# Performance work log

Hardware: AMD Instinct MI355X
Metric: run time of the kernel (lower is better)

Reference implementation:

```python
import jax, jax.numpy as jnp
import numpy as np

NUM_ATOMS = 4_000_000
NUM_TYPES = 11

def setup_inputs() -> dict:
    key = jax.random.key(0)
    k1, k2 = jax.random.split(key)
    input_coords = jax.random.normal(k1, (3 * NUM_ATOMS,), dtype=jnp.float32)
    atom_types = jax.random.randint(k2, (NUM_ATOMS,), 0, NUM_TYPES, dtype=jnp.int64)
    return {"input_coords": input_coords, "atom_types": atom_types, "num_atom_types": NUM_TYPES}

def reference(input_coords, atom_types, num_atom_types):
    # counts per atom type  [T]
    counts = jnp.bincount(atom_types, length=num_atom_types).astype(jnp.int32)
    # exclusive prefix sum -> bucket offsets  [T]
    offsets = (jnp.cumsum(counts) - counts).astype(jnp.int32)
    # stable sort by type reproduces the C++ bucket fill order:
    # atoms of the same type keep their original relative order.
    perm = jnp.argsort(atom_types, stable=True)  # [N] source index for each output slot
    coords3 = input_coords.reshape(-1, 3)        # [N,3]
    typed_coords = coords3[perm].reshape(-1)     # [3N] type-grouped flat coords
    return typed_coords, counts, offsets
```

## Files before the change

kernel.cpp:

```cpp
#include <hip/hip_runtime.h>

#define NTYPES 11
#define BLOCK  256
#define ITEMS  8
#define CHUNK  (BLOCK * ITEMS)
#define MAXCH  32

__global__ __launch_bounds__(BLOCK) void hist_kernel(
    const int* __restrict__ types, int N, int B, int* __restrict__ bc) {
  __shared__ int shCnt[NTYPES];
  const int tid = threadIdx.x;
  const int b = blockIdx.x;
  if (tid < NTYPES) shCnt[tid] = 0;
  __syncthreads();

  const int run = b * CHUNK + tid * ITEMS;
  int cnt[NTYPES];
#pragma unroll
  for (int t = 0; t < NTYPES; ++t) cnt[t] = 0;

  if (run < N) {
    const int4* p = (const int4*)(types + run);
    int4 a0 = p[0], a1 = p[1];
    int ty[ITEMS] = {a0.x, a0.y, a0.z, a0.w, a1.x, a1.y, a1.z, a1.w};
#pragma unroll
    for (int k = 0; k < ITEMS; ++k) {
#pragma unroll
      for (int t = 0; t < NTYPES; ++t) cnt[t] += (ty[k] == t) ? 1 : 0;
    }
  }

  const int lane = tid & 63;
#pragma unroll
  for (int t = 0; t < NTYPES; ++t) {
    int v = cnt[t];
    for (int o = 32; o >= 1; o >>= 1) v += __shfl_down(v, o);
    if (lane == 0) atomicAdd(&shCnt[t], v);
  }
  __syncthreads();
  if (tid < NTYPES) bc[tid * B + b] = shCnt[tid];
}

__global__ __launch_bounds__(NTYPES * 64) void scan_kernel(
    const int* __restrict__ bc, int B, int* __restrict__ scanOut,
    int* __restrict__ offs, float* __restrict__ outTail) {
  __shared__ int totals[NTYPES];
  const int lane = threadIdx.x & 63;
  const int t = threadIdx.x >> 6;
  const int nch = (B + 63) >> 6;

  int x[MAXCH];
#pragma unroll
  for (int c = 0; c < MAXCH; ++c) {
    const int idx = c * 64 + lane;
    x[c] = (c < nch && idx < B) ? bc[t * B + idx] : 0;
  }

  int carry = 0;
#pragma unroll
  for (int c = 0; c < MAXCH; ++c) {
    if (c >= nch) break;
    int incl = x[c];
#pragma unroll
    for (int o = 1; o < 64; o <<= 1) {
      int v = __shfl_up(incl, o);
      if (lane >= o) incl += v;
    }
    incl += carry;
    const int idx = c * 64 + lane;
    if (idx < B) scanOut[t * B + idx] = incl - x[c];
    carry = __shfl(incl, 63);
  }
  if (lane == 0) totals[t] = carry;
  __syncthreads();

  if (threadIdx.x == 0) {
    int off = 0;
    for (int u = 0; u < NTYPES; ++u) {
      const int c = totals[u];
      offs[u] = off;
      outTail[u] = (float)c;
      outTail[NTYPES + u] = (float)off;
      off += c;
    }
  }
}

__global__ __launch_bounds__(BLOCK) void scatter_kernel(
    const float* __restrict__ coords, const int* __restrict__ types,
    const int* __restrict__ scanOut, const int* __restrict__ offs, int N,
    int B, float* __restrict__ out) {
  __shared__ float shC[CHUNK * 3];
  __shared__ int wtot[NTYPES][4];
  __shared__ int shOff[NTYPES + 1];
  __shared__ int shDelta[NTYPES];

  const int tid = threadIdx.x;
  const int b = blockIdx.x;
  const int lane = tid & 63;
  const int wave = tid >> 6;
  const int run = b * CHUNK + tid * ITEMS;
  const bool active = (run < N);

  int ty[ITEMS];
  int cnt[NTYPES];
#pragma unroll
  for (int t = 0; t < NTYPES; ++t) cnt[t] = 0;
#pragma unroll
  for (int k = 0; k < ITEMS; ++k) ty[k] = -1;

  float c[ITEMS * 3];
  if (active) {
    const int4* p = (const int4*)(types + run);
    int4 a0 = p[0], a1 = p[1];
    int tt[ITEMS] = {a0.x, a0.y, a0.z, a0.w, a1.x, a1.y, a1.z, a1.w};
#pragma unroll
    for (int k = 0; k < ITEMS; ++k) ty[k] = tt[k];
    const float4* cp = (const float4*)(coords + (size_t)run * 3);
#pragma unroll
    for (int q = 0; q < (ITEMS * 3) / 4; ++q) {
      float4 v = cp[q];
      c[4 * q + 0] = v.x;
      c[4 * q + 1] = v.y;
      c[4 * q + 2] = v.z;
      c[4 * q + 3] = v.w;
    }
#pragma unroll
    for (int k = 0; k < ITEMS; ++k) {
#pragma unroll
      for (int t = 0; t < NTYPES; ++t) cnt[t] += (ty[k] == t) ? 1 : 0;
    }
  }

  int rank[NTYPES];
#pragma unroll
  for (int t = 0; t < NTYPES; ++t) {
    int incl = cnt[t];
#pragma unroll
    for (int o = 1; o < 64; o <<= 1) {
      int v = __shfl_up(incl, o);
      if (lane >= o) incl += v;
    }
    if (lane == 63) wtot[t][wave] = incl;
    rank[t] = incl - cnt[t];
  }
  __syncthreads();

  if (tid < NTYPES) {
    int loc = 0;
    for (int u = 0; u < tid; ++u)
      loc += wtot[u][0] + wtot[u][1] + wtot[u][2] + wtot[u][3];
    shOff[tid] = loc;
    shDelta[tid] = 3 * (offs[tid] + scanOut[tid * B + b] - loc);
    if (tid == NTYPES - 1) {
      shOff[NTYPES] =
          loc + wtot[tid][0] + wtot[tid][1] + wtot[tid][2] + wtot[tid][3];
    }
  }
  __syncthreads();

#pragma unroll
  for (int t = 0; t < NTYPES; ++t) {
    int wb = 0;
#pragma unroll
    for (int w = 0; w < 3; ++w) wb += (w < wave) ? wtot[t][w] : 0;
    rank[t] += wb + shOff[t];
  }

  if (active) {
#pragma unroll
    for (int k = 0; k < ITEMS; ++k) {
      const int t0 = ty[k];
      int slot = 0;
#pragma unroll
      for (int t = 0; t < NTYPES; ++t) {
        if (t0 == t) {
          slot = rank[t];
          rank[t] += 1;
        }
      }
      shC[3 * slot + 0] = c[3 * k + 0];
      shC[3 * slot + 1] = c[3 * k + 1];
      shC[3 * slot + 2] = c[3 * k + 2];
    }
  }
  __syncthreads();

  const int total = shOff[NTYPES];
  int offr[NTYPES];
  int dlt[NTYPES];
#pragma unroll
  for (int t = 0; t < NTYPES; ++t) {
    offr[t] = shOff[t];
    dlt[t] = shDelta[t];
  }
#pragma unroll
  for (int k = 0; k < ITEMS; ++k) {
    const int s = k * BLOCK + tid;
    if (s < total) {
      int d = dlt[0];
#pragma unroll
      for (int t = 1; t < NTYPES; ++t) d = (s >= offr[t]) ? dlt[t] : d;
      const int src = 3 * s;
      out[src + d + 0] = shC[src + 0];
      out[src + d + 1] = shC[src + 1];
      out[src + d + 2] = shC[src + 2];
    }
  }
}

extern "C" void kernel_launch(void* const* d_in, const int* in_sizes, int n_in,
                              void* d_out, int out_size, void* d_ws,
                              size_t ws_size, hipStream_t stream) {
  const float* coords = (const float*)d_in[0];
  const int* types = (const int*)d_in[1];
  const int N = in_sizes[1];
  const int B = (N + CHUNK - 1) / CHUNK;

  int* bc = (int*)d_ws;
  int* scanOut = bc + NTYPES * B;
  int* offs = scanOut + NTYPES * B;
  float* out = (float*)d_out;
  float* outTail = out + (size_t)3 * N;

  hist_kernel<<<B, BLOCK, 0, stream>>>(types, N, B, bc);
  scan_kernel<<<1, NTYPES * 64, 0, stream>>>(bc, B, scanOut, offs, outTail);
  scatter_kernel<<<B, BLOCK, 0, stream>>>(coords, types, scanOut, offs, N, B,
                                          out);
}
```

Baseline: 135.7 us.

## Fold global scan into scatter kernel with per-block redundant 16-bit count reduction

Removes the single-block scan kernel and its launch. Each scatter block now re-reads every block's per-type counts, stored as 16-bit values packed in pairs, and reduces them to get its own prefix and the global type offsets. The global write loop now stores one float per thread per step instead of three strided floats, which should coalesce better. The cost is that every block redundantly reads the whole count table (about 11*1954 shorts) and pays extra barriers, and the per-block counts must fit in 16 bits.

```diff
diff --git a/kernel.cpp b/kernel.cpp
--- a/kernel.cpp
+++ b/kernel.cpp
@@ -4,10 +4,10 @@
 #define BLOCK  256
 #define ITEMS  8
 #define CHUNK  (BLOCK * ITEMS)
-#define MAXCH  32
 
 __global__ __launch_bounds__(BLOCK) void hist_kernel(
-    const int* __restrict__ types, int N, int B, int* __restrict__ bc) {
+    const int* __restrict__ types, int N, int Bp,
+    unsigned short* __restrict__ bc) {
   __shared__ int shCnt[NTYPES];
   const int tid = threadIdx.x;
   const int b = blockIdx.x;
@@ -38,59 +38,18 @@
     if (lane == 0) atomicAdd(&shCnt[t], v);
   }
   __syncthreads();
-  if (tid < NTYPES) bc[tid * B + b] = shCnt[tid];
-}
-
-__global__ __launch_bounds__(NTYPES * 64) void scan_kernel(
-    const int* __restrict__ bc, int B, int* __restrict__ scanOut,
-    int* __restrict__ offs, float* __restrict__ outTail) {
-  __shared__ int totals[NTYPES];
-  const int lane = threadIdx.x & 63;
-  const int t = threadIdx.x >> 6;
-  const int nch = (B + 63) >> 6;
-
-  int x[MAXCH];
-#pragma unroll
-  for (int c = 0; c < MAXCH; ++c) {
-    const int idx = c * 64 + lane;
-    x[c] = (c < nch && idx < B) ? bc[t * B + idx] : 0;
-  }
-
-  int carry = 0;
-#pragma unroll
-  for (int c = 0; c < MAXCH; ++c) {
-    if (c >= nch) break;
-    int incl = x[c];
-#pragma unroll
-    for (int o = 1; o < 64; o <<= 1) {
-      int v = __shfl_up(incl, o);
-      if (lane >= o) incl += v;
-    }
-    incl += carry;
-    const int idx = c * 64 + lane;
-    if (idx < B) scanOut[t * B + idx] = incl - x[c];
-    carry = __shfl(incl, 63);
-  }
-  if (lane == 0) totals[t] = carry;
-  __syncthreads();
-
-  if (threadIdx.x == 0) {
-    int off = 0;
-    for (int u = 0; u < NTYPES; ++u) {
-      const int c = totals[u];
-      offs[u] = off;
-      outTail[u] = (float)c;
-      outTail[NTYPES + u] = (float)off;
-      off += c;
-    }
-  }
+  if (tid < NTYPES) bc[tid * Bp + b] = (unsigned short)shCnt[tid];
 }
 
 __global__ __launch_bounds__(BLOCK) void scatter_kernel(
     const float* __restrict__ coords, const int* __restrict__ types,
-    const int* __restrict__ scanOut, const int* __restrict__ offs, int N,
-    int B, float* __restrict__ out) {
+    const unsigned short* __restrict__ bc, int N, int B, int Bp,
+    float* __restrict__ out) {
   __shared__ float shC[CHUNK * 3];
+  __shared__ int red[NTYPES][2][4];
+  __shared__ int shPre[NTYPES];
+  __shared__ int shTot[NTYPES];
+  __shared__ int shGOff[NTYPES];
   __shared__ int wtot[NTYPES][4];
   __shared__ int shOff[NTYPES + 1];
   __shared__ int shDelta[NTYPES];
@@ -103,12 +62,8 @@
   const bool active = (run < N);
 
   int ty[ITEMS];
-  int cnt[NTYPES];
-#pragma unroll
-  for (int t = 0; t < NTYPES; ++t) cnt[t] = 0;
 #pragma unroll
   for (int k = 0; k < ITEMS; ++k) ty[k] = -1;
-
   float c[ITEMS * 3];
   if (active) {
     const int4* p = (const int4*)(types + run);
@@ -125,11 +80,73 @@
       c[4 * q + 2] = v.z;
       c[4 * q + 3] = v.w;
     }
-#pragma unroll
-    for (int k = 0; k < ITEMS; ++k) {
-#pragma unroll
-      for (int t = 0; t < NTYPES; ++t) cnt[t] += (ty[k] == t) ? 1 : 0;
-    }
+  }
+
+  const unsigned int* bc32 = (const unsigned int*)bc;
+  const int halfB = Bp >> 1;
+  int preAcc[NTYPES], totAcc[NTYPES];
+#pragma unroll
+  for (int t = 0; t < NTYPES; ++t) {
+    preAcc[t] = 0;
+    totAcc[t] = 0;
+  }
+  for (int i = tid; i < halfB; i += BLOCK) {
+    const int u0 = 2 * i;
+    const int u1 = 2 * i + 1;
+#pragma unroll
+    for (int t = 0; t < NTYPES; ++t) {
+      const unsigned int v = bc32[t * halfB + i];
+      int v0 = (int)(v & 0xFFFFu);
+      int v1 = (int)(v >> 16);
+      v1 = (u1 < B) ? v1 : 0;
+      totAcc[t] += v0 + v1;
+      preAcc[t] += ((u0 < b) ? v0 : 0) + ((u1 < b) ? v1 : 0);
+    }
+  }
+#pragma unroll
+  for (int t = 0; t < NTYPES; ++t) {
+    int p = preAcc[t], q = totAcc[t];
+    for (int o = 32; o >= 1; o >>= 1) {
+      p += __shfl_down(p, o);
+      q += __shfl_down(q, o);
+    }
+    if (lane == 0) {
+      red[t][0][wave] = p;
+      red[t][1][wave] = q;
+    }
+  }
+  __syncthreads();
+  if (tid < NTYPES) {
+    shPre[tid] = red[tid][0][0] + red[tid][0][1] + red[tid][0][2] + red[tid][0][3];
+    shTot[tid] = red[tid][1][0] + red[tid][1][1] + red[tid][1][2] + red[tid][1][3];
+  }
+  __syncthreads();
+  if (tid == 0) {
+    int off = 0;
+#pragma unroll
+    for (int t = 0; t < NTYPES; ++t) {
+      shGOff[t] = off;
+      off += shTot[t];
+    }
+  }
+  __syncthreads();
+
+  if (b == 0 && tid == 0) {
+    float* tail = out + (size_t)3 * N;
+#pragma unroll
+    for (int t = 0; t < NTYPES; ++t) {
+      tail[t] = (float)shTot[t];
+      tail[NTYPES + t] = (float)shGOff[t];
+    }
+  }
+
+  int cnt[NTYPES];
+#pragma unroll
+  for (int t = 0; t < NTYPES; ++t) cnt[t] = 0;
+#pragma unroll
+  for (int k = 0; k < ITEMS; ++k) {
+#pragma unroll
+    for (int t = 0; t < NTYPES; ++t) cnt[t] += (ty[k] == t) ? 1 : 0;
   }
 
   int rank[NTYPES];
@@ -151,7 +168,7 @@
     for (int u = 0; u < tid; ++u)
       loc += wtot[u][0] + wtot[u][1] + wtot[u][2] + wtot[u][3];
     shOff[tid] = loc;
-    shDelta[tid] = 3 * (offs[tid] + scanOut[tid * B + b] - loc);
+    shDelta[tid] = 3 * (shGOff[tid] + shPre[tid] - loc);
     if (tid == NTYPES - 1) {
       shOff[NTYPES] =
           loc + wtot[tid][0] + wtot[tid][1] + wtot[tid][2] + wtot[tid][3];
@@ -186,25 +203,22 @@
   }
   __syncthreads();
 
-  const int total = shOff[NTYPES];
-  int offr[NTYPES];
+  const int total3 = 3 * shOff[NTYPES];
+  int offr3[NTYPES];
   int dlt[NTYPES];
 #pragma unroll
   for (int t = 0; t < NTYPES; ++t) {
-    offr[t] = shOff[t];
+    offr3[t] = 3 * shOff[t];
     dlt[t] = shDelta[t];
   }
 #pragma unroll
-  for (int k = 0; k < ITEMS; ++k) {
-    const int s = k * BLOCK + tid;
-    if (s < total) {
+  for (int k = 0; k < ITEMS * 3; ++k) {
+    const int j = k * BLOCK + tid;
+    if (j < total3) {
       int d = dlt[0];
 #pragma unroll
-      for (int t = 1; t < NTYPES; ++t) d = (s >= offr[t]) ? dlt[t] : d;
-      const int src = 3 * s;
-      out[src + d + 0] = shC[src + 0];
-      out[src + d + 1] = shC[src + 1];
-      out[src + d + 2] = shC[src + 2];
+      for (int t = 1; t < NTYPES; ++t) d = (j >= offr3[t]) ? dlt[t] : d;
+      out[j + d] = shC[j];
     }
   }
 }
@@ -216,15 +230,11 @@
   const int* types = (const int*)d_in[1];
   const int N = in_sizes[1];
   const int B = (N + CHUNK - 1) / CHUNK;
-
-  int* bc = (int*)d_ws;
-  int* scanOut = bc + NTYPES * B;
-  int* offs = scanOut + NTYPES * B;
+  const int Bp = (B + 1) & ~1;
+
+  unsigned short* bc = (unsigned short*)d_ws;
   float* out = (float*)d_out;
-  float* outTail = out + (size_t)3 * N;
-
-  hist_kernel<<<B, BLOCK, 0, stream>>>(types, N, B, bc);
-  scan_kernel<<<1, NTYPES * 64, 0, stream>>>(bc, B, scanOut, offs, outTail);
-  scatter_kernel<<<B, BLOCK, 0, stream>>>(coords, types, scanOut, offs, N, B,
-                                          out);
+
+  hist_kernel<<<B, BLOCK, 0, stream>>>(types, N, Bp, bc);
+  scatter_kernel<<<B, BLOCK, 0, stream>>>(coords, types, bc, N, B, Bp, out);
 }
```

Result: slower. 157.5 us (+16.0%).

## Persistent scatter grid, packed 16-bit wave scan, and per-lane serial block scan

Applied to the files above, without the earlier changes.

The scatter kernel becomes a grid-stride persistent kernel capped at 1536 blocks instead of one block per chunk. Its per-type wave scans are packed two counts per 32-bit register, so 6 scans run instead of 11. The single-block scan kernel switches from chunked wave scans to a per-lane serial sum followed by one wave scan. Together these aim to cut shuffle count and launch/scheduling overhead, at the cost of an extra barrier per iteration and reliance on per-wave counts fitting in 16 bits.

```diff
diff --git a/kernel.cpp b/kernel.cpp
--- a/kernel.cpp
+++ b/kernel.cpp
@@ -4,7 +4,8 @@
 #define BLOCK  256
 #define ITEMS  8
 #define CHUNK  (BLOCK * ITEMS)
-#define MAXCH  32
+#define PERMAX 32
+#define SCATTER_GRID 1536
 
 __global__ __launch_bounds__(BLOCK) void hist_kernel(
     const int* __restrict__ types, int N, int B, int* __restrict__ bc) {
@@ -47,31 +48,35 @@
   __shared__ int totals[NTYPES];
   const int lane = threadIdx.x & 63;
   const int t = threadIdx.x >> 6;
-  const int nch = (B + 63) >> 6;
-
-  int x[MAXCH];
-#pragma unroll
-  for (int c = 0; c < MAXCH; ++c) {
-    const int idx = c * 64 + lane;
-    x[c] = (c < nch && idx < B) ? bc[t * B + idx] : 0;
-  }
-
-  int carry = 0;
-#pragma unroll
-  for (int c = 0; c < MAXCH; ++c) {
-    if (c >= nch) break;
-    int incl = x[c];
-#pragma unroll
-    for (int o = 1; o < 64; o <<= 1) {
-      int v = __shfl_up(incl, o);
-      if (lane >= o) incl += v;
-    }
-    incl += carry;
-    const int idx = c * 64 + lane;
-    if (idx < B) scanOut[t * B + idx] = incl - x[c];
-    carry = __shfl(incl, 63);
-  }
-  if (lane == 0) totals[t] = carry;
+  const int per = (B + 63) >> 6;
+  const int base = lane * per;
+
+  int x[PERMAX];
+#pragma unroll
+  for (int j = 0; j < PERMAX; ++j) {
+    const int idx = base + j;
+    x[j] = (j < per && idx < B) ? bc[t * B + idx] : 0;
+  }
+  int s = 0;
+#pragma unroll
+  for (int j = 0; j < PERMAX; ++j) s += x[j];
+
+  int incl = s;
+#pragma unroll
+  for (int o = 1; o < 64; o <<= 1) {
+    int v = __shfl_up(incl, o);
+    if (lane >= o) incl += v;
+  }
+  int run = incl - s;
+  const int total = __shfl(incl, 63);
+
+#pragma unroll
+  for (int j = 0; j < PERMAX; ++j) {
+    const int idx = base + j;
+    if (j < per && idx < B) scanOut[t * B + idx] = run;
+    run += x[j];
+  }
+  if (lane == 0) totals[t] = total;
   __syncthreads();
 
   if (threadIdx.x == 0) {
@@ -96,115 +101,135 @@
   __shared__ int shDelta[NTYPES];
 
   const int tid = threadIdx.x;
-  const int b = blockIdx.x;
   const int lane = tid & 63;
   const int wave = tid >> 6;
-  const int run = b * CHUNK + tid * ITEMS;
-  const bool active = (run < N);
-
-  int ty[ITEMS];
-  int cnt[NTYPES];
-#pragma unroll
-  for (int t = 0; t < NTYPES; ++t) cnt[t] = 0;
-#pragma unroll
-  for (int k = 0; k < ITEMS; ++k) ty[k] = -1;
-
-  float c[ITEMS * 3];
-  if (active) {
-    const int4* p = (const int4*)(types + run);
-    int4 a0 = p[0], a1 = p[1];
-    int tt[ITEMS] = {a0.x, a0.y, a0.z, a0.w, a1.x, a1.y, a1.z, a1.w};
-#pragma unroll
-    for (int k = 0; k < ITEMS; ++k) ty[k] = tt[k];
-    const float4* cp = (const float4*)(coords + (size_t)run * 3);
-#pragma unroll
-    for (int q = 0; q < (ITEMS * 3) / 4; ++q) {
-      float4 v = cp[q];
-      c[4 * q + 0] = v.x;
-      c[4 * q + 1] = v.y;
-      c[4 * q + 2] = v.z;
-      c[4 * q + 3] = v.w;
+
+  for (int b = blockIdx.x; b < B; b += gridDim.x) {
+    __syncthreads();
+
+    const int run = b * CHUNK + tid * ITEMS;
+    const bool active = (run < N);
+
+    int ty[ITEMS];
+    int cnt[NTYPES];
+#pragma unroll
+    for (int t = 0; t < NTYPES; ++t) cnt[t] = 0;
+#pragma unroll
+    for (int k = 0; k < ITEMS; ++k) ty[k] = -1;
+
+    float c[ITEMS * 3];
+    if (active) {
+      const int4* p = (const int4*)(types + run);
+      int4 a0 = p[0], a1 = p[1];
+      int tt[ITEMS] = {a0.x, a0.y, a0.z, a0.w, a1.x, a1.y, a1.z, a1.w};
+#pragma unroll
+      for (int k = 0; k < ITEMS; ++k) ty[k] = tt[k];
+      const float4* cp = (const float4*)(coords + (size_t)run * 3);
+#pragma unroll
+      for (int q = 0; q < (ITEMS * 3) / 4; ++q) {
+        float4 v = cp[q];
+        c[4 * q + 0] = v.x;
+        c[4 * q + 1] = v.y;
+        c[4 * q + 2] = v.z;
+        c[4 * q + 3] = v.w;
+      }
+#pragma unroll
+      for (int k = 0; k < ITEMS; ++k) {
+#pragma unroll
+        for (int t = 0; t < NTYPES; ++t) cnt[t] += (ty[k] == t) ? 1 : 0;
+      }
+    }
+
+    int pk[6];
+#pragma unroll
+    for (int q = 0; q < 5; ++q) pk[q] = cnt[2 * q] | (cnt[2 * q + 1] << 16);
+    pk[5] = cnt[10];
+#pragma unroll
+    for (int o = 1; o < 64; o <<= 1) {
+      int v0 = __shfl_up(pk[0], o);
+      int v1 = __shfl_up(pk[1], o);
+      int v2 = __shfl_up(pk[2], o);
+      int v3 = __shfl_up(pk[3], o);
+      int v4 = __shfl_up(pk[4], o);
+      int v5 = __shfl_up(pk[5], o);
+      if (lane >= o) {
+        pk[0] += v0;
+        pk[1] += v1;
+        pk[2] += v2;
+        pk[3] += v3;
+        pk[4] += v4;
+        pk[5] += v5;
+      }
+    }
+    int rank[NTYPES];
+#pragma unroll
+    for (int t = 0; t < NTYPES; ++t) {
+      const int incl = (pk[t >> 1] >> ((t & 1) * 16)) & 0xFFFF;
+      if (lane == 63) wtot[t][wave] = incl;
+      rank[t] = incl - cnt[t];
+    }
+    __syncthreads();
+
+    if (tid < NTYPES) {
+      int loc = 0;
+      for (int u = 0; u < tid; ++u)
+        loc += wtot[u][0] + wtot[u][1] + wtot[u][2] + wtot[u][3];
+      shOff[tid] = loc;
+      shDelta[tid] = 3 * (offs[tid] + scanOut[tid * B + b] - loc);
+      if (tid == NTYPES - 1) {
+        shOff[NTYPES] =
+            loc + wtot[tid][0] + wtot[tid][1] + wtot[tid][2] + wtot[tid][3];
+      }
+    }
+    __syncthreads();
+
+#pragma unroll
+    for (int t = 0; t < NTYPES; ++t) {
+      int wb = 0;
+#pragma unroll
+      for (int w = 0; w < 3; ++w) wb += (w < wave) ? wtot[t][w] : 0;
+      rank[t] += wb + shOff[t];
+    }
+
+    if (active) {
+#pragma unroll
+      for (int k = 0; k < ITEMS; ++k) {
+        const int t0 = ty[k];
+        int slot = 0;
+#pragma unroll
+        for (int t = 0; t < NTYPES; ++t) {
+          if (t0 == t) {
+            slot = rank[t];
+            rank[t] += 1;
+          }
+        }
+        shC[3 * slot + 0] = c[3 * k + 0];
+        shC[3 * slot + 1] = c[3 * k + 1];
+        shC[3 * slot + 2] = c[3 * k + 2];
+      }
+    }
+    __syncthreads();
+
+    const int total = shOff[NTYPES];
+    int offr[NTYPES];
+    int dlt[NTYPES];
+#pragma unroll
+    for (int t = 0; t < NTYPES; ++t) {
+      offr[t] = shOff[t];
+      dlt[t] = shDelta[t];
     }
 #pragma unroll
     for (int k = 0; k < ITEMS; ++k) {
-#pragma unroll
-      for (int t = 0; t < NTYPES; ++t) cnt[t] += (ty[k] == t) ? 1 : 0;
-    }
-  }
-
-  int rank[NTYPES];
-#pragma unroll
-  for (int t = 0; t < NTYPES; ++t) {
-    int incl = cnt[t];
-#pragma unroll
-    for (int o = 1; o < 64; o <<= 1) {
-      int v = __shfl_up(incl, o);
-      if (lane >= o) incl += v;
-    }
-    if (lane == 63) wtot[t][wave] = incl;
-    rank[t] = incl - cnt[t];
-  }
-  __syncthreads();
-
-  if (tid < NTYPES) {
-    int loc = 0;
-    for (int u = 0; u < tid; ++u)
-      loc += wtot[u][0] + wtot[u][1] + wtot[u][2] + wtot[u][3];
-    shOff[tid] = loc;
-    shDelta[tid] = 3 * (offs[tid] + scanOut[tid * B + b] - loc);
-    if (tid == NTYPES - 1) {
-      shOff[NTYPES] =
-          loc + wtot[tid][0] + wtot[tid][1] + wtot[tid][2] + wtot[tid][3];
-    }
-  }
-  __syncthreads();
-
-#pragma unroll
-  for (int t = 0; t < NTYPES; ++t) {
-    int wb = 0;
-#pragma unroll
-    for (int w = 0; w < 3; ++w) wb += (w < wave) ? wtot[t][w] : 0;
-    rank[t] += wb + shOff[t];
-  }
-
-  if (active) {
-#pragma unroll
-    for (int k = 0; k < ITEMS; ++k) {
-      const int t0 = ty[k];
-      int slot = 0;
-#pragma unroll
-      for (int t = 0; t < NTYPES; ++t) {
-        if (t0 == t) {
-          slot = rank[t];
-          rank[t] += 1;
-        }
-      }
-      shC[3 * slot + 0] = c[3 * k + 0];
-      shC[3 * slot + 1] = c[3 * k + 1];
-      shC[3 * slot + 2] = c[3 * k + 2];
-    }
-  }
-  __syncthreads();
-
-  const int total = shOff[NTYPES];
-  int offr[NTYPES];
-  int dlt[NTYPES];
-#pragma unroll
-  for (int t = 0; t < NTYPES; ++t) {
-    offr[t] = shOff[t];
-    dlt[t] = shDelta[t];
-  }
-#pragma unroll
-  for (int k = 0; k < ITEMS; ++k) {
-    const int s = k * BLOCK + tid;
-    if (s < total) {
-      int d = dlt[0];
-#pragma unroll
-      for (int t = 1; t < NTYPES; ++t) d = (s >= offr[t]) ? dlt[t] : d;
-      const int src = 3 * s;
-      out[src + d + 0] = shC[src + 0];
-      out[src + d + 1] = shC[src + 1];
-      out[src + d + 2] = shC[src + 2];
+      const int s = k * BLOCK + tid;
+      if (s < total) {
+        int d = dlt[0];
+#pragma unroll
+        for (int t = 1; t < NTYPES; ++t) d = (s >= offr[t]) ? dlt[t] : d;
+        const int src = 3 * s;
+        out[src + d + 0] = shC[src + 0];
+        out[src + d + 1] = shC[src + 1];
+        out[src + d + 2] = shC[src + 2];
+      }
     }
   }
 }
@@ -223,8 +248,10 @@
   float* out = (float*)d_out;
   float* outTail = out + (size_t)3 * N;
 
+  const int G = (B < SCATTER_GRID) ? B : SCATTER_GRID;
+
   hist_kernel<<<B, BLOCK, 0, stream>>>(types, N, B, bc);
   scan_kernel<<<1, NTYPES * 64, 0, stream>>>(bc, B, scanOut, offs, outTail);
-  scatter_kernel<<<B, BLOCK, 0, stream>>>(coords, types, scanOut, offs, N, B,
+  scatter_kernel<<<G, BLOCK, 0, stream>>>(coords, types, scanOut, offs, N, B,
                                           out);
 }
```

Measured after the change: 142.3 us. 4.9% more time.

## Pack atom types into 4-bit nibbles and vectorize scatter output writes

Applied to the files above, without the earlier changes.

The histogram kernel now writes the eight types each thread reads into one 32-bit word with 4 bits per type. The scatter kernel reads that word instead of re-reading the 32-byte type run, which cuts the second pass over the type array. The scatter write-out now reads float4 from shared memory and computes destination deltas per element group, with a fast path when all four floats fall in the same bucket. This adds an extra global write in the histogram pass and assumes types fit in 4 bits.

```diff
diff --git a/kernel.cpp b/kernel.cpp
--- a/kernel.cpp
+++ b/kernel.cpp
@@ -7,7 +7,8 @@
 #define MAXCH  32
 
 __global__ __launch_bounds__(BLOCK) void hist_kernel(
-    const int* __restrict__ types, int N, int B, int* __restrict__ bc) {
+    const int* __restrict__ types, int N, int B, int* __restrict__ bc,
+    unsigned int* __restrict__ packed) {
   __shared__ int shCnt[NTYPES];
   const int tid = threadIdx.x;
   const int b = blockIdx.x;
@@ -23,6 +24,10 @@
     const int4* p = (const int4*)(types + run);
     int4 a0 = p[0], a1 = p[1];
     int ty[ITEMS] = {a0.x, a0.y, a0.z, a0.w, a1.x, a1.y, a1.z, a1.w};
+    unsigned int pk = 0;
+#pragma unroll
+    for (int k = 0; k < ITEMS; ++k) pk |= ((unsigned int)ty[k]) << (4 * k);
+    packed[b * BLOCK + tid] = pk;
 #pragma unroll
     for (int k = 0; k < ITEMS; ++k) {
 #pragma unroll
@@ -87,7 +92,7 @@
 }
 
 __global__ __launch_bounds__(BLOCK) void scatter_kernel(
-    const float* __restrict__ coords, const int* __restrict__ types,
+    const float* __restrict__ coords, const unsigned int* __restrict__ packed,
     const int* __restrict__ scanOut, const int* __restrict__ offs, int N,
     int B, float* __restrict__ out) {
   __shared__ float shC[CHUNK * 3];
@@ -111,11 +116,9 @@
 
   float c[ITEMS * 3];
   if (active) {
-    const int4* p = (const int4*)(types + run);
-    int4 a0 = p[0], a1 = p[1];
-    int tt[ITEMS] = {a0.x, a0.y, a0.z, a0.w, a1.x, a1.y, a1.z, a1.w};
-#pragma unroll
-    for (int k = 0; k < ITEMS; ++k) ty[k] = tt[k];
+    const unsigned int pk = packed[b * BLOCK + tid];
+#pragma unroll
+    for (int k = 0; k < ITEMS; ++k) ty[k] = (int)((pk >> (4 * k)) & 0xFu);
     const float4* cp = (const float4*)(coords + (size_t)run * 3);
 #pragma unroll
     for (int q = 0; q < (ITEMS * 3) / 4; ++q) {
@@ -186,25 +189,44 @@
   }
   __syncthreads();
 
-  const int total = shOff[NTYPES];
-  int offr[NTYPES];
+  const int total3 = 3 * shOff[NTYPES];
+  int offr3[NTYPES];
   int dlt[NTYPES];
 #pragma unroll
   for (int t = 0; t < NTYPES; ++t) {
-    offr[t] = shOff[t];
+    offr3[t] = 3 * shOff[t];
     dlt[t] = shDelta[t];
   }
-#pragma unroll
-  for (int k = 0; k < ITEMS; ++k) {
-    const int s = k * BLOCK + tid;
-    if (s < total) {
-      int d = dlt[0];
-#pragma unroll
-      for (int t = 1; t < NTYPES; ++t) d = (s >= offr[t]) ? dlt[t] : d;
-      const int src = 3 * s;
-      out[src + d + 0] = shC[src + 0];
-      out[src + d + 1] = shC[src + 1];
-      out[src + d + 2] = shC[src + 2];
+  const float4* shC4 = (const float4*)shC;
+#pragma unroll
+  for (int k = 0; k < (ITEMS * 3) / 4; ++k) {
+    const int w = k * BLOCK + tid;
+    const int j0 = 4 * w;
+    if (j0 < total3) {
+      const float4 v = shC4[w];
+      int d0 = dlt[0], d3 = dlt[0];
+#pragma unroll
+      for (int t = 1; t < NTYPES; ++t) {
+        d0 = (j0 >= offr3[t]) ? dlt[t] : d0;
+        d3 = (j0 + 3 >= offr3[t]) ? dlt[t] : d3;
+      }
+      if (d0 == d3) {
+        out[j0 + d0 + 0] = v.x;
+        out[j0 + d0 + 1] = v.y;
+        out[j0 + d0 + 2] = v.z;
+        out[j0 + d0 + 3] = v.w;
+      } else {
+        int d1 = dlt[0], d2 = dlt[0];
+#pragma unroll
+        for (int t = 1; t < NTYPES; ++t) {
+          d1 = (j0 + 1 >= offr3[t]) ? dlt[t] : d1;
+          d2 = (j0 + 2 >= offr3[t]) ? dlt[t] : d2;
+        }
+        out[j0 + d0 + 0] = v.x;
+        out[j0 + d1 + 1] = v.y;
+        out[j0 + d2 + 2] = v.z;
+        out[j0 + d3 + 3] = v.w;
+      }
     }
   }
 }
@@ -220,11 +242,12 @@
   int* bc = (int*)d_ws;
   int* scanOut = bc + NTYPES * B;
   int* offs = scanOut + NTYPES * B;
+  unsigned int* packed = (unsigned int*)(offs + NTYPES + 1);
   float* out = (float*)d_out;
   float* outTail = out + (size_t)3 * N;
 
-  hist_kernel<<<B, BLOCK, 0, stream>>>(types, N, B, bc);
+  hist_kernel<<<B, BLOCK, 0, stream>>>(types, N, B, bc, packed);
   scan_kernel<<<1, NTYPES * 64, 0, stream>>>(bc, B, scanOut, offs, outTail);
-  scatter_kernel<<<B, BLOCK, 0, stream>>>(coords, types, scanOut, offs, N, B,
+  scatter_kernel<<<B, BLOCK, 0, stream>>>(coords, packed, scanOut, offs, N, B,
                                           out);
 }
```

New measurement: 137.3 us. No clear change (+1.2%).
